# Kernel optimization log

Measured on AMD Instinct MI355X. Metric: run time of the kernel, lower is better.

Reference implementation:

```python
import jax, jax.numpy as jnp
import numpy as np

OPTION_NUM = 5
HEADS = 4
NUM_LAYERS = 3
N_NODES = 20000
N_EDGES = 640000
NODES_PER_GRAPH = 800
N_GRAPHS = 25          # N_NODES // NODES_PER_GRAPH, multiple of OPTION_NUM
N_GROUPS = 5           # N_GRAPHS // OPTION_NUM; must equal OPTION_NUM for output_layer
T_TOK = 256
TOKEN_DIM = 1024
D = 256                # out_channels
VOCAB = 100000


def setup_inputs() -> dict:
    key = jax.random.key(0)
    ks = jax.random.split(key, 16)
    nrm = lambda k, s: jax.random.normal(k, s, dtype=jnp.float32) * 0.05
    L = NUM_LAYERS
    return {
        "concept_ids": jax.random.randint(ks[0], (N_NODES,), 0, VOCAB, dtype=jnp.int32),
        "edge_index": jax.random.randint(ks[1], (2, N_EDGES), 0, N_NODES, dtype=jnp.int32),
        "edge_type": jax.random.randint(ks[2], (N_EDGES,), 0, 38, dtype=jnp.int32),
        "sentence_embeddings": nrm(ks[3], (N_GROUPS, TOKEN_DIM)),
        "token_embedding": nrm(ks[4], (N_GROUPS, T_TOK, TOKEN_DIM)),
        "batch": (jnp.arange(N_NODES, dtype=jnp.int32) // NODES_PER_GRAPH),
        "entity_embeddings": nrm(ks[5], (VOCAB, D)),
        "Wq": nrm(ks[6], (L, D, D)), "bq": jnp.zeros((L, D), jnp.float32),
        "Wk": nrm(ks[7], (L, D, D)), "bk": jnp.zeros((L, D), jnp.float32),
        "Wv": nrm(ks[8], (L, D, D)), "bv": jnp.zeros((L, D), jnp.float32),
        "Ws": nrm(ks[9], (L, TOKEN_DIM, D)), "bs": jnp.zeros((L, D), jnp.float32),
        "Wo": nrm(ks[10], (L, D, D)), "bo": jnp.zeros((L, D), jnp.float32),
        "W1": nrm(ks[11], (D, D)), "b1": jnp.zeros((D,), jnp.float32),
        "W2": nrm(ks[12], (TOKEN_DIM, D)), "b2": jnp.zeros((D,), jnp.float32),
        "W3": nrm(ks[13], (D, TOKEN_DIM)), "b3": jnp.zeros((TOKEN_DIM,), jnp.float32),
        "Wout": nrm(ks[14], (OPTION_NUM * D, D)), "bout": jnp.zeros((D,), jnp.float32),
    }


def reference(concept_ids, edge_index, edge_type, sentence_embeddings, token_embedding,
              batch, entity_embeddings, Wq, bq, Wk, bk, Wv, bv, Ws, bs, Wo, bo,
              W1, b1, W2, b2, W3, b3, Wout, bout):
    H = HEADS
    C = D // H
    sqdk = jnp.sqrt(jnp.float32(C))
    group = batch // OPTION_NUM                      # [N] in [0, N_GROUPS)
    row, col = edge_index[0], edge_index[1]

    x = entity_embeddings[concept_ids]               # [N, D]
    for l in range(NUM_LAYERS):
        Q = (x @ Wq[l] + bq[l]).reshape(-1, H, C)
        K = (x @ Wk[l] + bk[l]).reshape(-1, H, C)
        V = (x @ Wv[l] + bv[l]).reshape(-1, H, C)
        QS = (sentence_embeddings[group] @ Ws[l] + bs[l]).reshape(-1, H, C)
        Qi, Kj = Q[row], K[col]                      # [E, H, C]
        alpha = ((Qi * Kj).sum(-1) + (QS[row] * Kj).sum(-1) + (Qi * QS[col]).sum(-1)) / (3.0 * sqdk)
        alpha = jax.nn.leaky_relu(alpha, 0.2)
        alpha = jax.nn.softmax(alpha, axis=0)        # global softmax over edges (as in source)
        agg = jnp.zeros_like(V).at[row].add(V[col] * alpha[:, :, None])
        x = agg.reshape(-1, H * C) @ Wo[l] + bo[l] + x

    x = x @ W1 + b1                                  # [N, D]
    tok = token_embedding @ W2 + b2                  # [G, T, D]

    # attention_multihead (faithful double gather by group indices)
    scale = jnp.sqrt(jnp.float32(D))
    scores = jnp.einsum('nd,btd->bnt', x, tok) / scale   # [G, N, T]
    sel = scores[:, group, :]                            # gather dim 1
    w = jax.nn.softmax(sel, axis=-1)
    ao = jnp.einsum('bnt,btd->bnd', w, tok)              # [G, N, D]
    sel2 = ao[:, group, :]                               # second gather
    concat = jnp.transpose(sel2, (1, 0, 2)).reshape(x.shape[0], -1)  # [N, G*D]
    x = concat @ Wout + bout                             # [N, D]

    pooled = jax.ops.segment_max(x, batch, num_segments=N_GRAPHS)    # global_max_pool
    soft = pooled @ W3 + b3                              # [N_GRAPHS, token_dim]
    return soft.reshape(N_GRAPHS // OPTION_NUM, OPTION_NUM, -1)
```

## Files before the change

kernel.cpp:

```cpp
#include <hip/hip_runtime.h>
#include <hip/hip_bf16.h>

#define NNODES 20000
#define NEDGES 640000
#define DM 256
#define PAD 128

typedef short s16x8 __attribute__((ext_vector_type(8)));
typedef float f32x4 __attribute__((ext_vector_type(4)));
typedef float f32x2 __attribute__((ext_vector_type(2)));

__device__ inline float b2f(unsigned short u) {
  union { unsigned int i; float f; } z;
  z.i = (unsigned int)u << 16;
  return z.f;
}
__device__ inline unsigned short f2b(float f) {
  union { unsigned int i; float f; } z;
  z.f = f;
  unsigned int i = z.i;
  return (unsigned short)((i + 0x7FFFu + ((i >> 16) & 1u)) >> 16);
}

__device__ inline unsigned char f2fp8(float v) {
#if __has_builtin(__builtin_amdgcn_cvt_pk_fp8_f32)
  int t = __builtin_amdgcn_cvt_pk_fp8_f32(v, v, 0, false);
  return (unsigned char)(t & 0xFF);
#else
  union { float f; unsigned int u; } z;
  z.f = v;
  unsigned int s = (z.u >> 31) << 7;
  float av = fabsf(v);
  if (av >= 448.f) return (unsigned char)(s | 0x7E);
  if (av < 0.015625f) {
    int q = (int)rintf(av * 512.f);
    return (unsigned char)(s | (unsigned)q);
  }
  int e32 = (int)((z.u >> 23) & 255) - 127;
  unsigned mant = z.u & 0x7FFFFF;
  unsigned t = mant + 0x7FFFF + ((mant >> 20) & 1);
  if (t >= 0x800000u) { t = 0; e32++; }
  int e4 = e32 + 7;
  unsigned m3 = (t >> 20) & 7;
  if (e4 > 15 || (e4 == 15 && m3 == 7)) return (unsigned char)(s | 0x7E);
  return (unsigned char)(s | (unsigned)((e4 << 3) | m3));
#endif
}

__device__ inline float4 fp8x4_dec(unsigned int u) {
#if __has_builtin(__builtin_amdgcn_cvt_pk_f32_fp8)
  f32x2 lo = __builtin_amdgcn_cvt_pk_f32_fp8((int)u, false);
  f32x2 hi = __builtin_amdgcn_cvt_pk_f32_fp8((int)u, true);
  float4 r;
  r.x = lo[0]; r.y = lo[1]; r.z = hi[0]; r.w = hi[1];
  return r;
#else
  float4 r;
  float* p = &r.x;
#pragma unroll
  for (int j = 0; j < 4; j++) {
    unsigned b = (u >> (8 * j)) & 0xFF;
    unsigned s = b >> 7, e = (b >> 3) & 15, m = b & 7;
    float mag;
    if (e == 0) mag = (float)m * 0.001953125f;
    else {
      union { unsigned int i; float f; } z;
      z.i = ((e + 120u) << 23) | (m << 20);
      mag = z.f;
    }
    p[j] = s ? -mag : mag;
  }
  return r;
#endif
}

__global__ __launch_bounds__(256) void gather_kernel(
    const int* __restrict__ cid, const float* __restrict__ ent,
    float* __restrict__ x, unsigned short* __restrict__ xb,
    int* __restrict__ deg, float* __restrict__ sums, int n) {
  int idx = blockIdx.x * 256 + threadIdx.x;
  if (idx < NNODES) deg[idx] = 0;
  if (idx < 12) sums[idx] = 0.f;
  if (idx >= n * 64) return;
  int node = idx >> 6, d4 = idx & 63;
  float4 v = reinterpret_cast<const float4*>(ent)[(size_t)cid[node] * 64 + d4];
  reinterpret_cast<float4*>(x)[(size_t)node * 64 + d4] = v;
  ushort4 b;
  b.x = f2b(v.x); b.y = f2b(v.y); b.z = f2b(v.z); b.w = f2b(v.w);
  reinterpret_cast<ushort4*>(xb)[(size_t)node * 64 + d4] = b;
}

__global__ __launch_bounds__(256) void prep_kernel(
    const float* __restrict__ Wq, const float* __restrict__ Wk,
    const float* __restrict__ Wv, const float* __restrict__ Wo,
    unsigned short* __restrict__ WT, const float* __restrict__ W2,
    unsigned short* __restrict__ W2T, const float* __restrict__ te,
    unsigned short* __restrict__ tb, const float* __restrict__ sent,
    const float* __restrict__ Ws, const float* __restrict__ bs,
    float* __restrict__ QS5all) {
  int blk = blockIdx.x;
  if (blk < 3072) {
    int slot = blk >> 8;
    int l = slot >> 2, t = slot & 3;
    int n = blk & 255;
    int k = threadIdx.x;
    const float* src = (t == 0) ? Wq : (t == 1) ? Wk : (t == 2) ? Wv : Wo;
    WT[(size_t)slot * 65536 + n * 256 + k] =
        f2b(src[(size_t)l * 65536 + k * 256 + n]);
  } else if (blk < 4096) {
    int i = (blk - 3072) * 256 + threadIdx.x;
    int n = i >> 10, k = i & 1023;
    W2T[n * 1024 + k] = f2b(W2[k * 256 + n]);
  } else if (blk < 5376) {
    int i = (blk - 4096) * 256 + threadIdx.x;
    float4 v = reinterpret_cast<const float4*>(te)[i];
    ushort4 b;
    b.x = f2b(v.x); b.y = f2b(v.y); b.z = f2b(v.z); b.w = f2b(v.w);
    reinterpret_cast<ushort4*>(tb)[i] = b;
  } else {
    int idx = blk - 5376;
    int g = idx % 5, l = idx / 5;
    int j = threadIdx.x;
    __shared__ float sh[1024];
    for (int i = j; i < 1024; i += 256) sh[i] = sent[g * 1024 + i];
    __syncthreads();
    const float* W = Ws + (size_t)l * 1024 * 256;
    float acc = bs[l * 256 + j];
    for (int k = 0; k < 1024; k++) acc += sh[k] * W[k * 256 + j];
    QS5all[(size_t)(l * 5 + g) * 256 + j] = acc;
  }
}

__global__ __launch_bounds__(256) void fill_kernel(const int* __restrict__ ei,
                                                   const int* __restrict__ batch,
                                                   int* __restrict__ deg,
                                                   int* __restrict__ colPad,
                                                   int E) {
  int e = blockIdx.x * 256 + threadIdx.x;
  if (e >= E) return;
  int r = ei[e];
  int c = ei[E + e];
  int slot = atomicAdd(&deg[r], 1);
  if (slot < PAD) colPad[(size_t)r * PAD + slot] = c | ((batch[c] / 5) << 24);
}

__global__ __launch_bounds__(256) void qkv_gemm_kernel(
    const unsigned short* __restrict__ A, const unsigned short* __restrict__ Bt,
    const float* __restrict__ bq, const float* __restrict__ bk,
    const float* __restrict__ bv, unsigned short* __restrict__ Qb,
    unsigned char* __restrict__ KV8, int M) {
  int wid = threadIdx.x >> 6;
  int lane = threadIdx.x & 63;
  int wr = wid >> 1, wc = wid & 1;
  int rowBase = blockIdx.y * 64 + wr * 32;
  int colBase = blockIdx.x * 128 + wc * 64;
  int r16 = lane & 15, kg = lane >> 4;
  f32x4 acc[2][4] = {};
  for (int k0 = 0; k0 < 256; k0 += 32) {
    s16x8 a[2], b[4];
#pragma unroll
    for (int mi = 0; mi < 2; mi++) {
      int r = rowBase + mi * 16 + r16;
      s16x8 z = {};
      a[mi] = (r < M) ? *reinterpret_cast<const s16x8*>(
                            &A[(size_t)r * 256 + k0 + kg * 8])
                      : z;
    }
#pragma unroll
    for (int ni = 0; ni < 4; ni++) {
      int c = colBase + ni * 16 + r16;
      b[ni] = *reinterpret_cast<const s16x8*>(&Bt[(size_t)c * 256 + k0 + kg * 8]);
    }
#pragma unroll
    for (int mi = 0; mi < 2; mi++)
#pragma unroll
      for (int ni = 0; ni < 4; ni++)
        acc[mi][ni] = __builtin_amdgcn_mfma_f32_16x16x32_bf16(
            a[mi], b[ni], acc[mi][ni], 0, 0, 0);
  }
  int region = (blockIdx.x * 128) >> 8;
  const float* bias = (region == 0) ? bq : (region == 1) ? bk : bv;
  unsigned char* dstBase = KV8 + ((region == 1) ? 0 : 256);
#pragma unroll
  for (int mi = 0; mi < 2; mi++)
#pragma unroll
    for (int ni = 0; ni < 4; ni++) {
      int cg = colBase + ni * 16 + (lane & 15);
      int cr = cg & 255;
      float bia = bias[cr];
#pragma unroll
      for (int reg = 0; reg < 4; reg++) {
        int r = rowBase + mi * 16 + (lane >> 4) * 4 + reg;
        if (r >= M) continue;
        float v = acc[mi][ni][reg] + bia;
        if (region == 0)
          Qb[(size_t)r * 256 + cr] = f2b(v);
        else
          dstBase[(size_t)r * 512 + cr] = f2fp8(v);
      }
    }
}

__global__ __launch_bounds__(256) void gemm_bf16_kernel(
    const unsigned short* __restrict__ A, const unsigned short* __restrict__ Bt,
    const float* __restrict__ bias, const float* __restrict__ resid,
    float* __restrict__ Cf, unsigned short* __restrict__ Cb, int M, int K) {
  int wid = threadIdx.x >> 6;
  int lane = threadIdx.x & 63;
  int wr = wid >> 1, wc = wid & 1;
  int rowBase = blockIdx.y * 64 + wr * 32;
  int colBase = blockIdx.x * 128 + wc * 64;
  int r16 = lane & 15, kg = lane >> 4;
  f32x4 acc[2][4] = {};
  for (int k0 = 0; k0 < K; k0 += 32) {
    s16x8 a[2], b[4];
#pragma unroll
    for (int mi = 0; mi < 2; mi++) {
      int r = rowBase + mi * 16 + r16;
      s16x8 z = {};
      a[mi] = (r < M) ? *reinterpret_cast<const s16x8*>(
                            &A[(size_t)r * K + k0 + kg * 8])
                      : z;
    }
#pragma unroll
    for (int ni = 0; ni < 4; ni++) {
      int c = colBase + ni * 16 + r16;
      b[ni] = *reinterpret_cast<const s16x8*>(&Bt[(size_t)c * K + k0 + kg * 8]);
    }
#pragma unroll
    for (int mi = 0; mi < 2; mi++)
#pragma unroll
      for (int ni = 0; ni < 4; ni++)
        acc[mi][ni] = __builtin_amdgcn_mfma_f32_16x16x32_bf16(
            a[mi], b[ni], acc[mi][ni], 0, 0, 0);
  }
#pragma unroll
  for (int mi = 0; mi < 2; mi++)
#pragma unroll
    for (int ni = 0; ni < 4; ni++) {
      int c = colBase + ni * 16 + (lane & 15);
      float bia = bias[c];
#pragma unroll
      for (int reg = 0; reg < 4; reg++) {
        int r = rowBase + mi * 16 + (lane >> 4) * 4 + reg;
        if (r >= M) continue;
        float v = acc[mi][ni][reg] + bia;
        if (resid) v += resid[(size_t)r * 256 + c];
        if (Cf) Cf[(size_t)r * 256 + c] = v;
        if (Cb) Cb[(size_t)r * 256 + c] = f2b(v);
      }
    }
}

__global__ __launch_bounds__(256) void rescale_wo_kernel(
    unsigned short* __restrict__ WoT, const float* __restrict__ sums) {
  int i = blockIdx.x * 256 + threadIdx.x;
  int head = (i & 255) >> 6;
  WoT[i] = f2b(b2f(WoT[i]) / sums[head]);
}

template <int DO_AGG>
__global__ __launch_bounds__(256) void fused_edge_kernel(
    const int* __restrict__ deg, const int* __restrict__ colPad,
    const int* __restrict__ batch, const unsigned short* __restrict__ Qb,
    const unsigned int* __restrict__ KV, const float* __restrict__ QS5,
    float* __restrict__ sums, unsigned short* __restrict__ aggb, int n) {
  int wv = __builtin_amdgcn_readfirstlane(threadIdx.x >> 6);
  int node = blockIdx.x * 4 + wv;
  int lane = threadIdx.x & 63;
  int head = lane >> 4;
  float sum0 = 0.f, sum1 = 0.f, sum2 = 0.f, sum3 = 0.f;
  float4 a0 = {0.f, 0.f, 0.f, 0.f}, a1 = a0, a2 = a0, a3 = a0;
  float4 qe = a0;
  float dq0 = 0.f, dq1 = 0.f, dq2 = 0.f, dq3 = 0.f, dq4 = 0.f;
  int dcount = 0;
  if (node < n) {
    ushort4 qu =
        reinterpret_cast<const ushort4*>(Qb)[(size_t)node * 64 + lane];
    float4 q = {b2f(qu.x), b2f(qu.y), b2f(qu.z), b2f(qu.w)};
    int gr = batch[node] / 5;
    float4 qs = reinterpret_cast<const float4*>(QS5)[gr * 64 + lane];
    qe.x = q.x + qs.x; qe.y = q.y + qs.y; qe.z = q.z + qs.z; qe.w = q.w + qs.w;
#pragma unroll
    for (int g = 0; g < 5; g++) {
      float4 w = reinterpret_cast<const float4*>(QS5)[g * 64 + lane];
      float d = q.x * w.x + q.y * w.y + q.z * w.z + q.w * w.w;
      d += __shfl_xor(d, 1);
      d += __shfl_xor(d, 2);
      d += __shfl_xor(d, 4);
      d += __shfl_xor(d, 8);
      if (g == 0) dq0 = d;
      else if (g == 1) dq1 = d;
      else if (g == 2) dq2 = d;
      else if (g == 3) dq3 = d;
      else dq4 = d;
    }
    dcount = deg[node];
    if (dcount > PAD) dcount = PAD;
  }
  const int* myCol = colPad + (size_t)node * PAD;
  bool lead = (lane & 15) == 0;
  int m = 0;
  for (; m + 4 <= dcount; m += 4) {
    int cc0 = myCol[m + 0], cc1 = myCol[m + 1];
    int cc2 = myCol[m + 2], cc3 = myCol[m + 3];
    int c0 = cc0 & 0xFFFFFF, c1 = cc1 & 0xFFFFFF;
    int c2 = cc2 & 0xFFFFFF, c3 = cc3 & 0xFFFFFF;
    unsigned int kr0 = KV[(size_t)c0 * 128 + lane];
    unsigned int kr1 = KV[(size_t)c1 * 128 + lane];
    unsigned int kr2 = KV[(size_t)c2 * 128 + lane];
    unsigned int kr3 = KV[(size_t)c3 * 128 + lane];
    unsigned int vr0 = 0, vr1 = 0, vr2 = 0, vr3 = 0;
    if (DO_AGG) {
      vr0 = KV[(size_t)c0 * 128 + 64 + lane];
      vr1 = KV[(size_t)c1 * 128 + 64 + lane];
      vr2 = KV[(size_t)c2 * 128 + 64 + lane];
      vr3 = KV[(size_t)c3 * 128 + 64 + lane];
    }
    float4 kd0 = fp8x4_dec(kr0), kd1 = fp8x4_dec(kr1);
    float4 kd2 = fp8x4_dec(kr2), kd3 = fp8x4_dec(kr3);
    float p0 = qe.x * kd0.x + qe.y * kd0.y + qe.z * kd0.z + qe.w * kd0.w;
    float p1 = qe.x * kd1.x + qe.y * kd1.y + qe.z * kd1.z + qe.w * kd1.w;
    float p2 = qe.x * kd2.x + qe.y * kd2.y + qe.z * kd2.z + qe.w * kd2.w;
    float p3 = qe.x * kd3.x + qe.y * kd3.y + qe.z * kd3.z + qe.w * kd3.w;
    p0 += __shfl_xor(p0, 1); p1 += __shfl_xor(p1, 1);
    p2 += __shfl_xor(p2, 1); p3 += __shfl_xor(p3, 1);
    p0 += __shfl_xor(p0, 2); p1 += __shfl_xor(p1, 2);
    p2 += __shfl_xor(p2, 2); p3 += __shfl_xor(p3, 2);
    p0 += __shfl_xor(p0, 4); p1 += __shfl_xor(p1, 4);
    p2 += __shfl_xor(p2, 4); p3 += __shfl_xor(p3, 4);
    p0 += __shfl_xor(p0, 8); p1 += __shfl_xor(p1, 8);
    p2 += __shfl_xor(p2, 8); p3 += __shfl_xor(p3, 8);
    int gc0 = cc0 >> 24, gc1 = cc1 >> 24, gc2 = cc2 >> 24, gc3 = cc3 >> 24;
    float dv0 = (gc0 == 0) ? dq0 : (gc0 == 1) ? dq1 : (gc0 == 2) ? dq2 : (gc0 == 3) ? dq3 : dq4;
    float dv1 = (gc1 == 0) ? dq0 : (gc1 == 1) ? dq1 : (gc1 == 2) ? dq2 : (gc1 == 3) ? dq3 : dq4;
    float dv2 = (gc2 == 0) ? dq0 : (gc2 == 1) ? dq1 : (gc2 == 2) ? dq2 : (gc2 == 3) ? dq3 : dq4;
    float dv3 = (gc3 == 0) ? dq0 : (gc3 == 1) ? dq1 : (gc3 == 2) ? dq2 : (gc3 == 3) ? dq3 : dq4;
    float v0 = (p0 + dv0) * (1.f / 24.f); v0 = (v0 >= 0.f) ? v0 : 0.2f * v0;
    float v1 = (p1 + dv1) * (1.f / 24.f); v1 = (v1 >= 0.f) ? v1 : 0.2f * v1;
    float v2 = (p2 + dv2) * (1.f / 24.f); v2 = (v2 >= 0.f) ? v2 : 0.2f * v2;
    float v3 = (p3 + dv3) * (1.f / 24.f); v3 = (v3 >= 0.f) ? v3 : 0.2f * v3;
    float e0 = __expf(v0), e1 = __expf(v1), e2 = __expf(v2), e3 = __expf(v3);
    if (lead) { sum0 += e0; sum1 += e1; sum2 += e2; sum3 += e3; }
    if (DO_AGG) {
      float4 vd0 = fp8x4_dec(vr0), vd1 = fp8x4_dec(vr1);
      float4 vd2 = fp8x4_dec(vr2), vd3 = fp8x4_dec(vr3);
      a0.x += e0 * vd0.x; a0.y += e0 * vd0.y; a0.z += e0 * vd0.z; a0.w += e0 * vd0.w;
      a1.x += e1 * vd1.x; a1.y += e1 * vd1.y; a1.z += e1 * vd1.z; a1.w += e1 * vd1.w;
      a2.x += e2 * vd2.x; a2.y += e2 * vd2.y; a2.z += e2 * vd2.z; a2.w += e2 * vd2.w;
      a3.x += e3 * vd3.x; a3.y += e3 * vd3.y; a3.z += e3 * vd3.z; a3.w += e3 * vd3.w;
    }
  }
  for (; m < dcount; m++) {
    int cc = myCol[m];
    int c = cc & 0xFFFFFF, gc = cc >> 24;
    float4 kd = fp8x4_dec(KV[(size_t)c * 128 + lane]);
    float p = qe.x * kd.x + qe.y * kd.y + qe.z * kd.z + qe.w * kd.w;
    p += __shfl_xor(p, 1);
    p += __shfl_xor(p, 2);
    p += __shfl_xor(p, 4);
    p += __shfl_xor(p, 8);
    float dqv = (gc == 0) ? dq0 : (gc == 1) ? dq1 : (gc == 2) ? dq2
                : (gc == 3) ? dq3 : dq4;
    float v = (p + dqv) * (1.f / 24.f);
    v = (v >= 0.f) ? v : 0.2f * v;
    float ev = __expf(v);
    if (lead) sum0 += ev;
    if (DO_AGG) {
      float4 vd = fp8x4_dec(KV[(size_t)c * 128 + 64 + lane]);
      a0.x += ev * vd.x; a0.y += ev * vd.y; a0.z += ev * vd.z; a0.w += ev * vd.w;
    }
  }
  float sumExp = (sum0 + sum1) + (sum2 + sum3);
  if (DO_AGG && node < n) {
    float4 acc;
    acc.x = (a0.x + a1.x) + (a2.x + a3.x);
    acc.y = (a0.y + a1.y) + (a2.y + a3.y);
    acc.z = (a0.z + a1.z) + (a2.z + a3.z);
    acc.w = (a0.w + a1.w) + (a2.w + a3.w);
    ushort4 b;
    b.x = f2b(acc.x); b.y = f2b(acc.y); b.z = f2b(acc.z); b.w = f2b(acc.w);
    reinterpret_cast<ushort4*>(aggb)[(size_t)node * 64 + lane] = b;
  }
  __shared__ float red[4][4];
  int w = threadIdx.x >> 6;
  if (lead) red[w][head] = sumExp;
  __syncthreads();
  if (threadIdx.x < 4) {
    float t = red[0][threadIdx.x] + red[1][threadIdx.x] + red[2][threadIdx.x] +
              red[3][threadIdx.x];
    atomicAdd(&sums[threadIdx.x], t);
  }
}

__global__ __launch_bounds__(1024) void tail_head_kernel(
    const int* __restrict__ deg, const int* __restrict__ colPad,
    const int* __restrict__ batch, const unsigned short* __restrict__ Qb,
    const unsigned int* __restrict__ KV, const unsigned short* __restrict__ xb,
    const float* __restrict__ QS5, const float* __restrict__ sums,
    const float* __restrict__ Wv2, const float* __restrict__ bv2,
    const float* __restrict__ Wo2, const float* __restrict__ bo2,
    const float* __restrict__ x, const float* __restrict__ W1,
    const float* __restrict__ b1, float* __restrict__ x1) {
  __shared__ float xh[4][256];
  __shared__ float sE4[4];
  __shared__ float a0s[256];
  __shared__ float t1[256];
  __shared__ float part[4][256];
  int tid = threadIdx.x;
  if (tid < 64) {
    int lane = tid;
    int head = lane >> 4;
    ushort4 qu = reinterpret_cast<const ushort4*>(Qb)[lane];
    float4 q = {b2f(qu.x), b2f(qu.y), b2f(qu.z), b2f(qu.w)};
    int gr = batch[0] / 5;
    float4 qs = reinterpret_cast<const float4*>(QS5)[gr * 64 + lane];
    float4 qe = {q.x + qs.x, q.y + qs.y, q.z + qs.z, q.w + qs.w};
    float dq0 = 0.f, dq1 = 0.f, dq2 = 0.f, dq3 = 0.f, dq4 = 0.f;
#pragma unroll
    for (int g = 0; g < 5; g++) {
      float4 w = reinterpret_cast<const float4*>(QS5)[g * 64 + lane];
      float d = q.x * w.x + q.y * w.y + q.z * w.z + q.w * w.w;
      d += __shfl_xor(d, 1);
      d += __shfl_xor(d, 2);
      d += __shfl_xor(d, 4);
      d += __shfl_xor(d, 8);
      if (g == 0) dq0 = d;
      else if (g == 1) dq1 = d;
      else if (g == 2) dq2 = d;
      else if (g == 3) dq3 = d;
      else dq4 = d;
    }
    float4 xaccA = {0, 0, 0, 0}, xaccB = xaccA, xaccC = xaccA, xaccD = xaccA;
    float sE = 0.f;
    int dcount = deg[0];
    if (dcount > PAD) dcount = PAD;
    for (int m = 0; m < dcount; m++) {
      int cc = colPad[m];
      int c = cc & 0xFFFFFF, gc = cc >> 24;
      float4 kd = fp8x4_dec(KV[(size_t)c * 128 + lane]);
      float p = qe.x * kd.x + qe.y * kd.y + qe.z * kd.z + qe.w * kd.w;
      p += __shfl_xor(p, 1);
      p += __shfl_xor(p, 2);
      p += __shfl_xor(p, 4);
      p += __shfl_xor(p, 8);
      float dqv = (gc == 0) ? dq0 : (gc == 1) ? dq1 : (gc == 2) ? dq2
                  : (gc == 3) ? dq3 : dq4;
      float v = (p + dqv) * (1.f / 24.f);
      v = (v >= 0.f) ? v : 0.2f * v;
      float ev = __expf(v);
      sE += ev;
      float e0 = __shfl(ev, 0);
      float e1 = __shfl(ev, 16);
      float e2 = __shfl(ev, 32);
      float e3 = __shfl(ev, 48);
      ushort4 xu = reinterpret_cast<const ushort4*>(xb)[(size_t)c * 64 + lane];
      float4 xv = {b2f(xu.x), b2f(xu.y), b2f(xu.z), b2f(xu.w)};
      xaccA.x += e0 * xv.x; xaccA.y += e0 * xv.y; xaccA.z += e0 * xv.z; xaccA.w += e0 * xv.w;
      xaccB.x += e1 * xv.x; xaccB.y += e1 * xv.y; xaccB.z += e1 * xv.z; xaccB.w += e1 * xv.w;
      xaccC.x += e2 * xv.x; xaccC.y += e2 * xv.y; xaccC.z += e2 * xv.z; xaccC.w += e2 * xv.w;
      xaccD.x += e3 * xv.x; xaccD.y += e3 * xv.y; xaccD.z += e3 * xv.z; xaccD.w += e3 * xv.w;
    }
    xh[0][lane * 4 + 0] = xaccA.x; xh[0][lane * 4 + 1] = xaccA.y;
    xh[0][lane * 4 + 2] = xaccA.z; xh[0][lane * 4 + 3] = xaccA.w;
    xh[1][lane * 4 + 0] = xaccB.x; xh[1][lane * 4 + 1] = xaccB.y;
    xh[1][lane * 4 + 2] = xaccB.z; xh[1][lane * 4 + 3] = xaccB.w;
    xh[2][lane * 4 + 0] = xaccC.x; xh[2][lane * 4 + 1] = xaccC.y;
    xh[2][lane * 4 + 2] = xaccC.z; xh[2][lane * 4 + 3] = xaccC.w;
    xh[3][lane * 4 + 0] = xaccD.x; xh[3][lane * 4 + 1] = xaccD.y;
    xh[3][lane * 4 + 2] = xaccD.z; xh[3][lane * 4 + 3] = xaccD.w;
    if ((lane & 15) == 0) sE4[head] = sE;
  }
  __syncthreads();
  int j = tid & 255, s = tid >> 8;
  int hj = j >> 6;
  float accv = 0.f;
#pragma unroll 8
  for (int k = s * 64; k < s * 64 + 64; k++) accv += xh[hj][k] * Wv2[k * 256 + j];
  part[s][j] = accv;
  __syncthreads();
  if (tid < 256) {
    float tot = part[0][tid] + part[1][tid] + part[2][tid] + part[3][tid] +
                sE4[hj] * bv2[tid];
    a0s[tid] = tot / sums[hj];
  }
  __syncthreads();
  float acc = 0.f;
#pragma unroll 8
  for (int k = s * 64; k < s * 64 + 64; k++) acc += a0s[k] * Wo2[k * 256 + j];
  part[s][j] = acc;
  __syncthreads();
  if (tid < 256)
    t1[tid] = part[0][tid] + part[1][tid] + part[2][tid] + part[3][tid] +
              bo2[tid] + x[tid];
  __syncthreads();
  float acc2 = 0.f;
#pragma unroll 8
  for (int k = s * 64; k < s * 64 + 64; k++) acc2 += t1[k] * W1[k * 256 + j];
  part[s][j] = acc2;
  __syncthreads();
  if (tid < 256)
    x1[tid] = part[0][tid] + part[1][tid] + part[2][tid] + part[3][tid] +
              b1[tid];
}

__global__ __launch_bounds__(256) void attn_out_kernel(
    const float* __restrict__ x1g, const float* __restrict__ tok,
    float* __restrict__ AO) {
  int b = blockIdx.x;
  int tid = threadIdx.x;
  int wave = tid >> 6, lane = tid & 63;
  int sub = lane >> 4, l16 = lane & 15;
  __shared__ float x1s[256];
  __shared__ float scs[256];
  __shared__ float red[256];
  __shared__ float wgt[256];
  x1s[tid] = x1g[tid];
  __syncthreads();
  const float4* xv4 = reinterpret_cast<const float4*>(x1s);
  for (int it = 0; it < 16; it++) {
    int row = wave * 64 + it * 4 + sub;
    const float4* tr =
        reinterpret_cast<const float4*>(tok + (size_t)(b * 256 + row) * 256);
    float sc = 0.f;
#pragma unroll
    for (int q = 0; q < 4; q++) {
      float4 v = tr[l16 + q * 16];
      float4 xv = xv4[l16 + q * 16];
      sc += v.x * xv.x + v.y * xv.y + v.z * xv.z + v.w * xv.w;
    }
    sc += __shfl_xor(sc, 1);
    sc += __shfl_xor(sc, 2);
    sc += __shfl_xor(sc, 4);
    sc += __shfl_xor(sc, 8);
    if (l16 == 0) scs[row] = sc * (1.f / 16.f);
  }
  __syncthreads();
  float sc = scs[tid];
  red[tid] = sc;
  __syncthreads();
  for (int off = 128; off; off >>= 1) {
    if (tid < off) red[tid] = fmaxf(red[tid], red[tid + off]);
    __syncthreads();
  }
  float mx = red[0];
  __syncthreads();
  float ex = expf(sc - mx);
  red[tid] = ex;
  __syncthreads();
  for (int off = 128; off; off >>= 1) {
    if (tid < off) red[tid] += red[tid + off];
    __syncthreads();
  }
  wgt[tid] = ex / red[0];
  __syncthreads();
  float acc = 0.f;
#pragma unroll 4
  for (int k = 0; k < 256; k++)
    acc += wgt[k] * tok[(size_t)(b * 256 + k) * 256 + tid];
  AO[b * 256 + tid] = acc;
}

__global__ __launch_bounds__(256) void final_y_kernel(
    const float* __restrict__ AO, const float* __restrict__ Wout,
    float* __restrict__ partial) {
  int s = blockIdx.x;
  int j = threadIdx.x;
  __shared__ float a[80];
  if (threadIdx.x < 80) a[threadIdx.x] = AO[s * 80 + threadIdx.x];
  __syncthreads();
  const float* W = Wout + (size_t)s * 80 * 256;
  float acc = 0.f;
#pragma unroll 8
  for (int k = 0; k < 80; k++) acc += a[k] * W[k * 256 + j];
  partial[s * 256 + j] = acc;
}

__global__ __launch_bounds__(256) void final_out2_kernel(
    const float* __restrict__ partial, const float* __restrict__ bout,
    const float* __restrict__ W3, const float* __restrict__ b3,
    float* __restrict__ out) {
  __shared__ float y[256];
  int j = threadIdx.x;
  float acc = bout[j];
#pragma unroll
  for (int s = 0; s < 16; s++) acc += partial[s * 256 + j];
  y[j] = acc;
  __syncthreads();
  int t = blockIdx.x * 256 + j;
  float o = b3[t];
#pragma unroll 8
  for (int k = 0; k < 256; k++) o += y[k] * W3[k * 1024 + t];
  for (int g = 0; g < 25; g++) out[(size_t)g * 1024 + t] = o;
}

extern "C" void kernel_launch(void* const* d_in, const int* in_sizes, int n_in,
                              void* d_out, int out_size, void* d_ws,
                              size_t ws_size, hipStream_t stream) {
  const int* concept_ids = (const int*)d_in[0];
  const int* edge_index = (const int*)d_in[1];
  const float* sent = (const float*)d_in[3];
  const float* tokemb = (const float*)d_in[4];
  const int* batch = (const int*)d_in[5];
  const float* ent = (const float*)d_in[6];
  const float* Wq = (const float*)d_in[7];
  const float* bq = (const float*)d_in[8];
  const float* Wk = (const float*)d_in[9];
  const float* bk = (const float*)d_in[10];
  const float* Wv = (const float*)d_in[11];
  const float* bv = (const float*)d_in[12];
  const float* Ws = (const float*)d_in[13];
  const float* bs = (const float*)d_in[14];
  const float* Wo = (const float*)d_in[15];
  const float* bo = (const float*)d_in[16];
  const float* W1 = (const float*)d_in[17];
  const float* b1 = (const float*)d_in[18];
  const float* W2 = (const float*)d_in[19];
  const float* b2 = (const float*)d_in[20];
  const float* W3 = (const float*)d_in[21];
  const float* b3 = (const float*)d_in[22];
  const float* Wout = (const float*)d_in[23];
  const float* bout = (const float*)d_in[24];
  float* out = (float*)d_out;

  float* ws = (float*)d_ws;
  size_t off_ = 0;
  auto alloc = [&](size_t n) {
    float* p = ws + off_;
    off_ += n;
    return p;
  };
  float* x = alloc((size_t)NNODES * DM);
  float* x2 = alloc((size_t)NNODES * DM);
  unsigned short* Qb = (unsigned short*)alloc((size_t)NNODES * DM / 2);
  unsigned short* xb = (unsigned short*)alloc((size_t)NNODES * DM / 2);
  unsigned short* aggb = (unsigned short*)alloc((size_t)NNODES * DM / 2);
  unsigned char* KV8 = (unsigned char*)alloc((size_t)NNODES * DM / 2);
  unsigned short* WT = (unsigned short*)alloc(12 * 65536 / 2);
  unsigned short* W2T = (unsigned short*)alloc(262144 / 2);
  unsigned short* tokb = (unsigned short*)alloc(1280 * 1024 / 2);
  float* tok = alloc(1280 * 256);
  float* QS5all = alloc(3 * 5 * 256);
  float* sums = alloc(16);
  float* x1 = alloc(256);
  float* AO = alloc(1280);
  float* partial = alloc(16 * 256);
  int* deg = (int*)alloc(NNODES);
  int* colPad = (int*)alloc((size_t)NNODES * PAD);

  gather_kernel<<<5000, 256, 0, stream>>>(concept_ids, ent, x, xb, deg, sums,
                                          NNODES);
  prep_kernel<<<5391, 256, 0, stream>>>(Wq, Wk, Wv, Wo, WT, W2, W2T, tokemb,
                                        tokb, sent, Ws, bs, QS5all);
  fill_kernel<<<(NEDGES + 255) / 256, 256, 0, stream>>>(edge_index, batch, deg,
                                                        colPad, NEDGES);

  float* xin = x;
  float* xout = x2;
  for (int l = 0; l < 3; l++) {
    unsigned short* WoT = WT + (size_t)(l * 4 + 3) * 65536;
    {
      dim3 g((l < 2) ? 6 : 4, (NNODES + 63) / 64);
      qkv_gemm_kernel<<<g, 256, 0, stream>>>(
          xb, WT + (size_t)(l * 4) * 65536, bq + l * DM, bk + l * DM,
          bv + l * DM, Qb, KV8, NNODES);
    }
    if (l < 2) {
      fused_edge_kernel<1><<<5000, 256, 0, stream>>>(
          deg, colPad, batch, Qb, (const unsigned int*)KV8, QS5all + l * 1280,
          sums + l * 4, aggb, NNODES);
      rescale_wo_kernel<<<256, 256, 0, stream>>>(WoT, sums + l * 4);
      dim3 g(2, (NNODES + 63) / 64);
      gemm_bf16_kernel<<<g, 256, 0, stream>>>(aggb, WoT, bo + l * DM, xin,
                                              xout, xb, NNODES, 256);
      float* tmp = xin;
      xin = xout;
      xout = tmp;
    } else {
      fused_edge_kernel<0><<<5000, 256, 0, stream>>>(
          deg, colPad, batch, Qb, (const unsigned int*)KV8, QS5all + l * 1280,
          sums + l * 4, nullptr, NNODES);
      tail_head_kernel<<<1, 1024, 0, stream>>>(
          deg, colPad, batch, Qb, (const unsigned int*)KV8, xb,
          QS5all + l * 1280, sums + l * 4, Wv + (size_t)2 * 65536,
          bv + 2 * DM, Wo + (size_t)2 * 65536, bo + 2 * DM, xin, W1, b1, x1);
    }
  }

  {
    dim3 g(2, 1280 / 64);
    gemm_bf16_kernel<<<g, 256, 0, stream>>>(tokb, W2T, b2, nullptr, tok,
                                            nullptr, 1280, 1024);
  }
  attn_out_kernel<<<5, 256, 0, stream>>>(x1, tok, AO);
  final_y_kernel<<<16, 256, 0, stream>>>(AO, Wout, partial);
  final_out2_kernel<<<4, 256, 0, stream>>>(partial, bout, W3, b3, out);
}
```

Measured before the change: 618.7 us.

## Merge setup kernels into one launch and fold token GEMM into layer-0 QKV

The gather, weight-prep and edge-fill kernels become one init_kernel that dispatches on block index. The deg and sums buffers are now zeroed with memsets beforehand. The token projection GEMM is folded into the layer-0 QKV GEMM as extra column blocks, so it overlaps with the QKV work instead of running as its own small launch at the end. LeakyReLU is rewritten as fmaxf(v, 0.2v). The aim is fewer launches and less serialization of small kernels, at the cost of more branching inside each kernel and a mixed workload within one grid.

```diff
diff --git a/kernel.cpp b/kernel.cpp
--- a/kernel.cpp
+++ b/kernel.cpp
@@ -74,87 +74,127 @@
 #endif
 }
 
-__global__ __launch_bounds__(256) void gather_kernel(
+__global__ __launch_bounds__(256) void init_kernel(
     const int* __restrict__ cid, const float* __restrict__ ent,
     float* __restrict__ x, unsigned short* __restrict__ xb,
-    int* __restrict__ deg, float* __restrict__ sums, int n) {
-  int idx = blockIdx.x * 256 + threadIdx.x;
-  if (idx < NNODES) deg[idx] = 0;
-  if (idx < 12) sums[idx] = 0.f;
-  if (idx >= n * 64) return;
-  int node = idx >> 6, d4 = idx & 63;
-  float4 v = reinterpret_cast<const float4*>(ent)[(size_t)cid[node] * 64 + d4];
-  reinterpret_cast<float4*>(x)[(size_t)node * 64 + d4] = v;
-  ushort4 b;
-  b.x = f2b(v.x); b.y = f2b(v.y); b.z = f2b(v.z); b.w = f2b(v.w);
-  reinterpret_cast<ushort4*>(xb)[(size_t)node * 64 + d4] = b;
-}
-
-__global__ __launch_bounds__(256) void prep_kernel(
     const float* __restrict__ Wq, const float* __restrict__ Wk,
     const float* __restrict__ Wv, const float* __restrict__ Wo,
     unsigned short* __restrict__ WT, const float* __restrict__ W2,
     unsigned short* __restrict__ W2T, const float* __restrict__ te,
     unsigned short* __restrict__ tb, const float* __restrict__ sent,
     const float* __restrict__ Ws, const float* __restrict__ bs,
-    float* __restrict__ QS5all) {
+    float* __restrict__ QS5all, const int* __restrict__ ei,
+    const int* __restrict__ batch, int* __restrict__ deg,
+    int* __restrict__ colPad) {
   int blk = blockIdx.x;
-  if (blk < 3072) {
-    int slot = blk >> 8;
-    int l = slot >> 2, t = slot & 3;
-    int n = blk & 255;
-    int k = threadIdx.x;
-    const float* src = (t == 0) ? Wq : (t == 1) ? Wk : (t == 2) ? Wv : Wo;
-    WT[(size_t)slot * 65536 + n * 256 + k] =
-        f2b(src[(size_t)l * 65536 + k * 256 + n]);
-  } else if (blk < 4096) {
-    int i = (blk - 3072) * 256 + threadIdx.x;
-    int n = i >> 10, k = i & 1023;
-    W2T[n * 1024 + k] = f2b(W2[k * 256 + n]);
-  } else if (blk < 5376) {
-    int i = (blk - 4096) * 256 + threadIdx.x;
-    float4 v = reinterpret_cast<const float4*>(te)[i];
+  if (blk < 5000) {
+    int idx = blk * 256 + threadIdx.x;
+    if (idx >= NNODES * 64) return;
+    int node = idx >> 6, d4 = idx & 63;
+    float4 v =
+        reinterpret_cast<const float4*>(ent)[(size_t)cid[node] * 64 + d4];
+    reinterpret_cast<float4*>(x)[(size_t)node * 64 + d4] = v;
     ushort4 b;
     b.x = f2b(v.x); b.y = f2b(v.y); b.z = f2b(v.z); b.w = f2b(v.w);
-    reinterpret_cast<ushort4*>(tb)[i] = b;
+    reinterpret_cast<ushort4*>(xb)[(size_t)node * 64 + d4] = b;
+  } else if (blk < 10391) {
+    int pblk = blk - 5000;
+    if (pblk < 3072) {
+      int slot = pblk >> 8;
+      int l = slot >> 2, t = slot & 3;
+      int n = pblk & 255;
+      int k = threadIdx.x;
+      const float* src = (t == 0) ? Wq : (t == 1) ? Wk : (t == 2) ? Wv : Wo;
+      WT[(size_t)slot * 65536 + n * 256 + k] =
+          f2b(src[(size_t)l * 65536 + k * 256 + n]);
+    } else if (pblk < 4096) {
+      int i = (pblk - 3072) * 256 + threadIdx.x;
+      int n = i >> 10, k = i & 1023;
+      W2T[n * 1024 + k] = f2b(W2[k * 256 + n]);
+    } else if (pblk < 5376) {
+      int i = (pblk - 4096) * 256 + threadIdx.x;
+      float4 v = reinterpret_cast<const float4*>(te)[i];
+      ushort4 b;
+      b.x = f2b(v.x); b.y = f2b(v.y); b.z = f2b(v.z); b.w = f2b(v.w);
+      reinterpret_cast<ushort4*>(tb)[i] = b;
+    } else {
+      int idx = pblk - 5376;
+      int g = idx % 5, l = idx / 5;
+      int j = threadIdx.x;
+      __shared__ float sh[1024];
+      for (int i = j; i < 1024; i += 256) sh[i] = sent[g * 1024 + i];
+      __syncthreads();
+      const float* W = Ws + (size_t)l * 1024 * 256;
+      float acc = bs[l * 256 + j];
+      for (int k = 0; k < 1024; k++) acc += sh[k] * W[k * 256 + j];
+      QS5all[(size_t)(l * 5 + g) * 256 + j] = acc;
+    }
   } else {
-    int idx = blk - 5376;
-    int g = idx % 5, l = idx / 5;
-    int j = threadIdx.x;
-    __shared__ float sh[1024];
-    for (int i = j; i < 1024; i += 256) sh[i] = sent[g * 1024 + i];
-    __syncthreads();
-    const float* W = Ws + (size_t)l * 1024 * 256;
-    float acc = bs[l * 256 + j];
-    for (int k = 0; k < 1024; k++) acc += sh[k] * W[k * 256 + j];
-    QS5all[(size_t)(l * 5 + g) * 256 + j] = acc;
-  }
-}
-
-__global__ __launch_bounds__(256) void fill_kernel(const int* __restrict__ ei,
-                                                   const int* __restrict__ batch,
-                                                   int* __restrict__ deg,
-                                                   int* __restrict__ colPad,
-                                                   int E) {
-  int e = blockIdx.x * 256 + threadIdx.x;
-  if (e >= E) return;
-  int r = ei[e];
-  int c = ei[E + e];
-  int slot = atomicAdd(&deg[r], 1);
-  if (slot < PAD) colPad[(size_t)r * PAD + slot] = c | ((batch[c] / 5) << 24);
-}
-
+    int e = (blk - 10391) * 256 + threadIdx.x;
+    if (e >= NEDGES) return;
+    int r = ei[e];
+    int c = ei[NEDGES + e];
+    int slot = atomicAdd(&deg[r], 1);
+    if (slot < PAD)
+      colPad[(size_t)r * PAD + slot] = c | ((batch[c] / 5) << 24);
+  }
+}
+
+template <int WITH_TOK>
 __global__ __launch_bounds__(256) void qkv_gemm_kernel(
     const unsigned short* __restrict__ A, const unsigned short* __restrict__ Bt,
     const float* __restrict__ bq, const float* __restrict__ bk,
     const float* __restrict__ bv, unsigned short* __restrict__ Qb,
-    unsigned char* __restrict__ KV8, int M) {
+    unsigned char* __restrict__ KV8, int M,
+    const unsigned short* __restrict__ tokA,
+    const unsigned short* __restrict__ W2T, const float* __restrict__ b2,
+    float* __restrict__ tokOut) {
   int wid = threadIdx.x >> 6;
   int lane = threadIdx.x & 63;
   int wr = wid >> 1, wc = wid & 1;
+  int r16 = lane & 15, kg = lane >> 4;
+  if (WITH_TOK && blockIdx.x >= 6) {
+    if (blockIdx.y >= 20) return;
+    int rowBase = blockIdx.y * 64 + wr * 32;
+    int colBase = (blockIdx.x - 6) * 128 + wc * 64;
+    f32x4 acc[2][4] = {};
+    for (int k0 = 0; k0 < 1024; k0 += 32) {
+      s16x8 a[2], b[4];
+#pragma unroll
+      for (int mi = 0; mi < 2; mi++) {
+        int r = rowBase + mi * 16 + r16;
+        a[mi] = *reinterpret_cast<const s16x8*>(
+            &tokA[(size_t)r * 1024 + k0 + kg * 8]);
+      }
+#pragma unroll
+      for (int ni = 0; ni < 4; ni++) {
+        int c = colBase + ni * 16 + r16;
+        b[ni] = *reinterpret_cast<const s16x8*>(
+            &W2T[(size_t)c * 1024 + k0 + kg * 8]);
+      }
+#pragma unroll
+      for (int mi = 0; mi < 2; mi++)
+#pragma unroll
+        for (int ni = 0; ni < 4; ni++)
+          acc[mi][ni] = __builtin_amdgcn_mfma_f32_16x16x32_bf16(
+              a[mi], b[ni], acc[mi][ni], 0, 0, 0);
+    }
+#pragma unroll
+    for (int mi = 0; mi < 2; mi++)
+#pragma unroll
+      for (int ni = 0; ni < 4; ni++) {
+        int c = colBase + ni * 16 + (lane & 15);
+        float bia = b2[c];
+#pragma unroll
+        for (int reg = 0; reg < 4; reg++) {
+          int r = rowBase + mi * 16 + (lane >> 4) * 4 + reg;
+          tokOut[(size_t)r * 256 + c] = acc[mi][ni][reg] + bia;
+        }
+      }
+    return;
+  }
   int rowBase = blockIdx.y * 64 + wr * 32;
   int colBase = blockIdx.x * 128 + wc * 64;
-  int r16 = lane & 15, kg = lane >> 4;
   f32x4 acc[2][4] = {};
   for (int k0 = 0; k0 < 256; k0 += 32) {
     s16x8 a[2], b[4];
@@ -336,10 +376,10 @@
     float dv1 = (gc1 == 0) ? dq0 : (gc1 == 1) ? dq1 : (gc1 == 2) ? dq2 : (gc1 == 3) ? dq3 : dq4;
     float dv2 = (gc2 == 0) ? dq0 : (gc2 == 1) ? dq1 : (gc2 == 2) ? dq2 : (gc2 == 3) ? dq3 : dq4;
     float dv3 = (gc3 == 0) ? dq0 : (gc3 == 1) ? dq1 : (gc3 == 2) ? dq2 : (gc3 == 3) ? dq3 : dq4;
-    float v0 = (p0 + dv0) * (1.f / 24.f); v0 = (v0 >= 0.f) ? v0 : 0.2f * v0;
-    float v1 = (p1 + dv1) * (1.f / 24.f); v1 = (v1 >= 0.f) ? v1 : 0.2f * v1;
-    float v2 = (p2 + dv2) * (1.f / 24.f); v2 = (v2 >= 0.f) ? v2 : 0.2f * v2;
-    float v3 = (p3 + dv3) * (1.f / 24.f); v3 = (v3 >= 0.f) ? v3 : 0.2f * v3;
+    float v0 = (p0 + dv0) * (1.f / 24.f); v0 = fmaxf(v0, 0.2f * v0);
+    float v1 = (p1 + dv1) * (1.f / 24.f); v1 = fmaxf(v1, 0.2f * v1);
+    float v2 = (p2 + dv2) * (1.f / 24.f); v2 = fmaxf(v2, 0.2f * v2);
+    float v3 = (p3 + dv3) * (1.f / 24.f); v3 = fmaxf(v3, 0.2f * v3);
     float e0 = __expf(v0), e1 = __expf(v1), e2 = __expf(v2), e3 = __expf(v3);
     if (lead) { sum0 += e0; sum1 += e1; sum2 += e2; sum3 += e3; }
     if (DO_AGG) {
@@ -363,7 +403,7 @@
     float dqv = (gc == 0) ? dq0 : (gc == 1) ? dq1 : (gc == 2) ? dq2
                 : (gc == 3) ? dq3 : dq4;
     float v = (p + dqv) * (1.f / 24.f);
-    v = (v >= 0.f) ? v : 0.2f * v;
+    v = fmaxf(v, 0.2f * v);
     float ev = __expf(v);
     if (lead) sum0 += ev;
     if (DO_AGG) {
@@ -447,7 +487,7 @@
       float dqv = (gc == 0) ? dq0 : (gc == 1) ? dq1 : (gc == 2) ? dq2
                   : (gc == 3) ? dq3 : dq4;
       float v = (p + dqv) * (1.f / 24.f);
-      v = (v >= 0.f) ? v : 0.2f * v;
+      v = fmaxf(v, 0.2f * v);
       float ev = __expf(v);
       sE += ev;
       float e0 = __shfl(ev, 0);
@@ -648,22 +688,26 @@
   int* deg = (int*)alloc(NNODES);
   int* colPad = (int*)alloc((size_t)NNODES * PAD);
 
-  gather_kernel<<<5000, 256, 0, stream>>>(concept_ids, ent, x, xb, deg, sums,
-                                          NNODES);
-  prep_kernel<<<5391, 256, 0, stream>>>(Wq, Wk, Wv, Wo, WT, W2, W2T, tokemb,
-                                        tokb, sent, Ws, bs, QS5all);
-  fill_kernel<<<(NEDGES + 255) / 256, 256, 0, stream>>>(edge_index, batch, deg,
-                                                        colPad, NEDGES);
+  hipMemsetAsync(deg, 0, NNODES * sizeof(int), stream);
+  hipMemsetAsync(sums, 0, 12 * sizeof(float), stream);
+  init_kernel<<<12891, 256, 0, stream>>>(
+      concept_ids, ent, x, xb, Wq, Wk, Wv, Wo, WT, W2, W2T, tokemb, tokb, sent,
+      Ws, bs, QS5all, edge_index, batch, deg, colPad);
 
   float* xin = x;
   float* xout = x2;
   for (int l = 0; l < 3; l++) {
     unsigned short* WoT = WT + (size_t)(l * 4 + 3) * 65536;
-    {
+    if (l == 0) {
+      dim3 g(8, (NNODES + 63) / 64);
+      qkv_gemm_kernel<1><<<g, 256, 0, stream>>>(
+          xb, WT + (size_t)(l * 4) * 65536, bq + l * DM, bk + l * DM,
+          bv + l * DM, Qb, KV8, NNODES, tokb, W2T, b2, tok);
+    } else {
       dim3 g((l < 2) ? 6 : 4, (NNODES + 63) / 64);
-      qkv_gemm_kernel<<<g, 256, 0, stream>>>(
+      qkv_gemm_kernel<0><<<g, 256, 0, stream>>>(
           xb, WT + (size_t)(l * 4) * 65536, bq + l * DM, bk + l * DM,
-          bv + l * DM, Qb, KV8, NNODES);
+          bv + l * DM, Qb, KV8, NNODES, nullptr, nullptr, nullptr, nullptr);
     }
     if (l < 2) {
       fused_edge_kernel<1><<<5000, 256, 0, stream>>>(
@@ -687,11 +731,6 @@
     }
   }
 
-  {
-    dim3 g(2, 1280 / 64);
-    gemm_bf16_kernel<<<g, 256, 0, stream>>>(tokb, W2T, b2, nullptr, tok,
-                                            nullptr, 1280, 1024);
-  }
   attn_out_kernel<<<5, 256, 0, stream>>>(x1, tok, AO);
   final_y_kernel<<<16, 256, 0, stream>>>(AO, Wout, partial);
   final_out2_kernel<<<4, 256, 0, stream>>>(partial, bout, W3, b3, out);
```

Measured after the change: 606.1 us. -2.0%, faster.
